# Optimization experiments

Hardware: AMD Instinct MI355X
Metric: run time of the kernel (lower is better)

The kernel has to match this reference:

```python
import jax, jax.numpy as jnp
import numpy as np

N_NODES = 50000
N_EDGES = 800000
FEAT = 128
HID1 = 128
HID2 = 64


def setup_inputs() -> dict:
    key = jax.random.key(0)
    k = jax.random.split(key, 6)
    x = jax.random.normal(k[0], (N_NODES, FEAT), dtype=jnp.float32)
    edge_index = jax.random.randint(k[1], (2, N_EDGES), 0, N_NODES, dtype=jnp.int32)
    # Glorot-style init scaling like PyG's GCNConv linear
    W1 = jax.random.normal(k[2], (FEAT, HID1), dtype=jnp.float32) * (1.0 / np.sqrt(FEAT))
    b1 = jnp.zeros((HID1,), dtype=jnp.float32)
    W2 = jax.random.normal(k[3], (HID1, HID2), dtype=jnp.float32) * (1.0 / np.sqrt(HID1))
    b2 = jnp.zeros((HID2,), dtype=jnp.float32)
    return {"x": x, "edge_index": edge_index, "W1": W1, "b1": b1, "W2": W2, "b2": b2}


def _gcn_conv(x, src, dst, W, b, n_nodes):
    """PyG GCNConv: h = X W; out_i = sum_j norm_ij h_j + b, with self-loops and
    symmetric normalization norm_ij = deg_i^-1/2 * deg_j^-1/2 (deg counts self-loop)."""
    h = x @ W  # [N, out]
    # degree at target nodes (self-loops already appended to src/dst)
    deg = jax.ops.segment_sum(jnp.ones_like(dst, dtype=h.dtype), dst, num_segments=n_nodes)
    dinv = jax.lax.rsqrt(jnp.maximum(deg, 1.0))  # deg >= 1 because of self-loops
    norm = dinv[src] * dinv[dst]  # [E+N]
    msg = h[src] * norm[:, None]  # gather + scale, [E+N, out]
    out = jax.ops.segment_sum(msg, dst, num_segments=n_nodes)
    return out + b


def reference(x, edge_index, W1, b1, W2, b2):
    n = x.shape[0]
    self_idx = jnp.arange(n, dtype=edge_index.dtype)
    src = jnp.concatenate([edge_index[0], self_idx])
    dst = jnp.concatenate([edge_index[1], self_idx])
    h = jax.nn.relu(_gcn_conv(x, src, dst, W1, b1, n))
    out = _gcn_conv(h, src, dst, W2, b2, n)
    return out
```

## Files before the change

kernel.cpp:

```cpp
#include <hip/hip_runtime.h>
#include <hip/hip_bf16.h>


__device__ __forceinline__ float bf_lo(unsigned u) { return __uint_as_float(u << 16); }
__device__ __forceinline__ float bf_hi(unsigned u) { return __uint_as_float(u & 0xffff0000u); }
__device__ __forceinline__ unsigned short f2bf(float f) {
    return (unsigned short)(__bfloat16_as_ushort(__float2bfloat16(f)));
}

__global__ __launch_bounds__(256) void zero_kernel(int* __restrict__ a, int n) {
    int i = blockIdx.x * 256 + threadIdx.x;
    if (i < n) a[i] = 0;
}

__global__ __launch_bounds__(256) void count_kernel(const int* __restrict__ dst,
                                                    int* __restrict__ cnt,
                                                    int* __restrict__ eslot, int E) {
    int e = blockIdx.x * 256 + threadIdx.x;
    if (e < E) eslot[e] = atomicAdd(&cnt[dst[e]], 1);
}

__global__ __launch_bounds__(256) void scan1_kernel(const int* __restrict__ cnt,
                                                    int* __restrict__ row_ptr,
                                                    int* __restrict__ blksum,
                                                    float* __restrict__ dinv, int N) {
    __shared__ int sm[256];
    int i = blockIdx.x * 256 + threadIdx.x;
    int v = (i < N) ? cnt[i] : 0;
    if (i < N) dinv[i] = rsqrtf((float)(v + 1));
    sm[threadIdx.x] = v;
    __syncthreads();
    for (int off = 1; off < 256; off <<= 1) {
        int t = (threadIdx.x >= off) ? sm[threadIdx.x - off] : 0;
        __syncthreads();
        sm[threadIdx.x] += t;
        __syncthreads();
    }
    if (i < N) row_ptr[i] = sm[threadIdx.x] - v;
    if (threadIdx.x == 255) blksum[blockIdx.x] = sm[255];
}

__global__ __launch_bounds__(256) void scan2_kernel(int* __restrict__ blksum, int nb) {
    __shared__ int sm[256];
    int i = threadIdx.x;
    int v = (i < nb) ? blksum[i] : 0;
    sm[i] = v;
    __syncthreads();
    for (int off = 1; off < 256; off <<= 1) {
        int t = (i >= off) ? sm[i - off] : 0;
        __syncthreads();
        sm[i] += t;
        __syncthreads();
    }
    if (i < nb) blksum[i] = sm[i] - v;
}

__global__ __launch_bounds__(256) void scan3_kernel(int* __restrict__ row_ptr,
                                                    const int* __restrict__ blksum,
                                                    int N, int E) {
    int i = blockIdx.x * 256 + threadIdx.x;
    if (i < N) row_ptr[i] += blksum[blockIdx.x];
    if (i == 0) row_ptr[N] = E;
}

__global__ __launch_bounds__(256) void scatter_kernel(const int* __restrict__ src,
                                                      const int* __restrict__ dst,
                                                      const int* __restrict__ row_ptr,
                                                      const int* __restrict__ eslot,
                                                      int* __restrict__ ssrc, int E) {
    int e = blockIdx.x * 256 + threadIdx.x;
    if (e < E) {
        int p = row_ptr[dst[e]] + eslot[e];
        ssrc[p] = src[e];
    }
}

template <int M>
__global__ __launch_bounds__(256) void gemm_kernel(const float* __restrict__ A,
                                                   const float* __restrict__ W,
                                                   const float* __restrict__ dinv,
                                                   unsigned short* __restrict__ C,
                                                   int N) {
    constexpr int K = 128, KC = 32, TN = M / 16;
    __shared__ float As[64][33];
    __shared__ float Bs[KC][M];

    int tid = threadIdx.x;
    int tx = tid & 15;
    int ty = tid >> 4;
    int row0 = blockIdx.x * 64;

    float acc[4][TN];
#pragma unroll
    for (int i = 0; i < 4; ++i)
#pragma unroll
        for (int j = 0; j < TN; ++j) acc[i][j] = 0.f;

    for (int kc = 0; kc < K; kc += KC) {
#pragma unroll
        for (int f = 0; f < 2; ++f) {
            int q = tid + 256 * f;
            int r = q >> 3;
            int kq = (q & 7) << 2;
            int grow = row0 + r;
            float4 v = make_float4(0.f, 0.f, 0.f, 0.f);
            if (grow < N) v = *(const float4*)(A + (size_t)grow * K + kc + kq);
            As[r][kq + 0] = v.x;
            As[r][kq + 1] = v.y;
            As[r][kq + 2] = v.z;
            As[r][kq + 3] = v.w;
        }
        constexpr int BQ = KC * M / 4;
#pragma unroll
        for (int f = 0; f < BQ / 256; ++f) {
            int q = tid + 256 * f;
            int r = q / (M / 4);
            int c4 = (q % (M / 4)) << 2;
            *(float4*)(&Bs[r][c4]) = *(const float4*)(W + (size_t)(kc + r) * M + c4);
        }
        __syncthreads();

#pragma unroll
        for (int k = 0; k < KC; ++k) {
            float a[4], b[TN];
#pragma unroll
            for (int i = 0; i < 4; ++i) a[i] = As[ty * 4 + i][k];
#pragma unroll
            for (int j = 0; j < TN; ++j) b[j] = Bs[k][tx * TN + j];
#pragma unroll
            for (int i = 0; i < 4; ++i)
#pragma unroll
                for (int j = 0; j < TN; ++j) acc[i][j] += a[i] * b[j];
        }
        __syncthreads();
    }

#pragma unroll
    for (int i = 0; i < 4; ++i) {
        int grow = row0 + ty * 4 + i;
        if (grow < N) {
            float dv = dinv[grow];
            unsigned short us[TN];
#pragma unroll
            for (int j = 0; j < TN; ++j) us[j] = f2bf(acc[i][j] * dv);
            if constexpr (TN == 8) {
                uint4 pk;
                pk.x = (unsigned)us[0] | ((unsigned)us[1] << 16);
                pk.y = (unsigned)us[2] | ((unsigned)us[3] << 16);
                pk.z = (unsigned)us[4] | ((unsigned)us[5] << 16);
                pk.w = (unsigned)us[6] | ((unsigned)us[7] << 16);
                *(uint4*)(C + (size_t)grow * M + tx * TN) = pk;
            } else {
                uint2 pk;
                pk.x = (unsigned)us[0] | ((unsigned)us[1] << 16);
                pk.y = (unsigned)us[2] | ((unsigned)us[3] << 16);
                *(uint2*)(C + (size_t)grow * M + tx * TN) = pk;
            }
        }
    }
}

template <int M, bool RELU>
__global__ __launch_bounds__(256) void agg_kernel(const unsigned short* __restrict__ g,
                                                  const int* __restrict__ row_ptr,
                                                  const int* __restrict__ ssrc,
                                                  const float* __restrict__ dinv,
                                                  const float* __restrict__ bias,
                                                  float* __restrict__ out, int N) {
    int node = __builtin_amdgcn_readfirstlane((int)(blockIdx.x * 4 + (threadIdx.x >> 6)));
    if (node >= N) return;
    int lane = threadIdx.x & 63;
    float di = dinv[node];
    int beg = row_ptr[node];
    int end = row_ptr[node + 1];

    if constexpr (M == 128) {
        const unsigned* hp = (const unsigned*)g;
        unsigned hv = hp[node * 64 + lane];
        float ax0 = bf_lo(hv), ay0 = bf_hi(hv);
        float ax1 = 0.f, ay1 = 0.f;
        int j = beg;
        for (; j + 7 < end; j += 8) {
            int s0 = ssrc[j + 0], s1 = ssrc[j + 1], s2 = ssrc[j + 2], s3 = ssrc[j + 3];
            int s4 = ssrc[j + 4], s5 = ssrc[j + 5], s6 = ssrc[j + 6], s7 = ssrc[j + 7];
            unsigned v0 = hp[s0 * 64 + lane], v1 = hp[s1 * 64 + lane];
            unsigned v2 = hp[s2 * 64 + lane], v3 = hp[s3 * 64 + lane];
            unsigned v4 = hp[s4 * 64 + lane], v5 = hp[s5 * 64 + lane];
            unsigned v6 = hp[s6 * 64 + lane], v7 = hp[s7 * 64 + lane];
            ax0 += bf_lo(v0) + bf_lo(v1) + bf_lo(v2) + bf_lo(v3);
            ax1 += bf_lo(v4) + bf_lo(v5) + bf_lo(v6) + bf_lo(v7);
            ay0 += bf_hi(v0) + bf_hi(v1) + bf_hi(v2) + bf_hi(v3);
            ay1 += bf_hi(v4) + bf_hi(v5) + bf_hi(v6) + bf_hi(v7);
        }
        for (; j + 3 < end; j += 4) {
            int s0 = ssrc[j + 0], s1 = ssrc[j + 1], s2 = ssrc[j + 2], s3 = ssrc[j + 3];
            unsigned v0 = hp[s0 * 64 + lane], v1 = hp[s1 * 64 + lane];
            unsigned v2 = hp[s2 * 64 + lane], v3 = hp[s3 * 64 + lane];
            ax0 += bf_lo(v0) + bf_lo(v1);
            ax1 += bf_lo(v2) + bf_lo(v3);
            ay0 += bf_hi(v0) + bf_hi(v1);
            ay1 += bf_hi(v2) + bf_hi(v3);
        }
        for (; j < end; ++j) {
            unsigned v = hp[ssrc[j] * 64 + lane];
            ax0 += bf_lo(v);
            ay0 += bf_hi(v);
        }
        float ax = (ax0 + ax1) * di + bias[2 * lane];
        float ay = (ay0 + ay1) * di + bias[2 * lane + 1];
        if (RELU) { ax = fmaxf(ax, 0.f); ay = fmaxf(ay, 0.f); }
        ((float2*)out)[node * 64 + lane] = make_float2(ax, ay);
    } else {
        float a0 = __uint_as_float((unsigned)g[node * 64 + lane] << 16);
        float a1 = 0.f;
        int j = beg;
        for (; j + 7 < end; j += 8) {
            int s0 = ssrc[j + 0], s1 = ssrc[j + 1], s2 = ssrc[j + 2], s3 = ssrc[j + 3];
            int s4 = ssrc[j + 4], s5 = ssrc[j + 5], s6 = ssrc[j + 6], s7 = ssrc[j + 7];
            float v0 = __uint_as_float((unsigned)g[s0 * 64 + lane] << 16);
            float v1 = __uint_as_float((unsigned)g[s1 * 64 + lane] << 16);
            float v2 = __uint_as_float((unsigned)g[s2 * 64 + lane] << 16);
            float v3 = __uint_as_float((unsigned)g[s3 * 64 + lane] << 16);
            float v4 = __uint_as_float((unsigned)g[s4 * 64 + lane] << 16);
            float v5 = __uint_as_float((unsigned)g[s5 * 64 + lane] << 16);
            float v6 = __uint_as_float((unsigned)g[s6 * 64 + lane] << 16);
            float v7 = __uint_as_float((unsigned)g[s7 * 64 + lane] << 16);
            a0 += v0 + v1 + v2 + v3;
            a1 += v4 + v5 + v6 + v7;
        }
        for (; j + 3 < end; j += 4) {
            int s0 = ssrc[j + 0], s1 = ssrc[j + 1], s2 = ssrc[j + 2], s3 = ssrc[j + 3];
            float v0 = __uint_as_float((unsigned)g[s0 * 64 + lane] << 16);
            float v1 = __uint_as_float((unsigned)g[s1 * 64 + lane] << 16);
            float v2 = __uint_as_float((unsigned)g[s2 * 64 + lane] << 16);
            float v3 = __uint_as_float((unsigned)g[s3 * 64 + lane] << 16);
            a0 += v0 + v1;
            a1 += v2 + v3;
        }
        for (; j < end; ++j)
            a0 += __uint_as_float((unsigned)g[ssrc[j] * 64 + lane] << 16);
        float acc = (a0 + a1) * di + bias[lane];
        if (RELU) acc = fmaxf(acc, 0.f);
        out[node * 64 + lane] = acc;
    }
}

extern "C" void kernel_launch(void* const* d_in, const int* in_sizes, int n_in,
                              void* d_out, int out_size, void* d_ws, size_t ws_size,
                              hipStream_t stream) {
    const float* x = (const float*)d_in[0];
    const int* eidx = (const int*)d_in[1];
    const float* W1 = (const float*)d_in[2];
    const float* b1 = (const float*)d_in[3];
    const float* W2 = (const float*)d_in[4];
    const float* b2 = (const float*)d_in[5];
    float* out = (float*)d_out;

    const int N = in_sizes[0] / 128;
    const int E = in_sizes[1] / 2;
    const int* src = eidx;
    const int* dst = eidx + E;

    char* ws = (char*)d_ws;
    size_t off = 0;
    auto alloc = [&](size_t bytes) -> char* {
        char* p = ws + off;
        off = (off + bytes + 255) & ~(size_t)255;
        return p;
    };
    int* cnt = (int*)alloc((size_t)N * 4);
    int* row_ptr = (int*)alloc((size_t)(N + 1) * 4);
    int* blksum = (int*)alloc(256 * 4);
    int* eslot = (int*)alloc((size_t)E * 4);
    int* ssrc = (int*)alloc((size_t)E * 4);
    float* dinv = (float*)alloc((size_t)N * 4);
    unsigned short* g1 = (unsigned short*)alloc((size_t)N * 128 * 2);
    float* z1 = (float*)alloc((size_t)N * 128 * 4);
    unsigned short* g2 = (unsigned short*)alloc((size_t)N * 64 * 2);

    const int nbN = (N + 255) / 256;
    const int nbE = (E + 255) / 256;

    zero_kernel<<<nbN, 256, 0, stream>>>(cnt, N);
    count_kernel<<<nbE, 256, 0, stream>>>(dst, cnt, eslot, E);
    scan1_kernel<<<nbN, 256, 0, stream>>>(cnt, row_ptr, blksum, dinv, N);
    scan2_kernel<<<1, 256, 0, stream>>>(blksum, nbN);
    scan3_kernel<<<nbN, 256, 0, stream>>>(row_ptr, blksum, N, E);
    scatter_kernel<<<nbE, 256, 0, stream>>>(src, dst, row_ptr, eslot, ssrc, E);

    const int gb = (N + 63) / 64;
    gemm_kernel<128><<<gb, 256, 0, stream>>>(x, W1, dinv, g1, N);
    agg_kernel<128, true><<<(N + 3) / 4, 256, 0, stream>>>(g1, row_ptr, ssrc, dinv, b1, z1, N);
    gemm_kernel<64><<<gb, 256, 0, stream>>>(z1, W2, dinv, g2, N);
    agg_kernel<64, false><<<(N + 3) / 4, 256, 0, stream>>>(g2, row_ptr, ssrc, dinv, b2, out, N);
}
```

Before: 233.1 us.

## Store layer-1 activations in bf16 and restructure GEMM with full-row A tiles

The first aggregation now writes its ReLU output as bf16 instead of fp32, halving the intermediate buffer that the second GEMM reads. The GEMM loads the whole 64x128 A tile into shared memory once, as fp32 or bf16, instead of per K-chunk. Its inner loop is rewritten to use float4 shared-memory reads with an interleaved column mapping for vectorized B access. This trades extra rounding of the hidden activations for less memory traffic, and the larger shared footprint (32KB for fp32 A) may reduce occupancy.

New measurement: 243.7 us. 1.05x slower.

```diff
diff --git a/kernel.cpp b/kernel.cpp
--- a/kernel.cpp
+++ b/kernel.cpp
@@ -75,41 +75,55 @@
     }
 }
 
-template <int M>
-__global__ __launch_bounds__(256) void gemm_kernel(const float* __restrict__ A,
+template <int M, bool ABF16>
+__global__ __launch_bounds__(256) void gemm_kernel(const void* __restrict__ Araw,
                                                    const float* __restrict__ W,
                                                    const float* __restrict__ dinv,
                                                    unsigned short* __restrict__ C,
                                                    int N) {
-    constexpr int K = 128, KC = 32, TN = M / 16;
-    __shared__ float As[64][33];
+    constexpr int K = 128, KC = 32, TN = M / 16, NH = M / 64;
     __shared__ float Bs[KC][M];
-
-    int tid = threadIdx.x;
-    int tx = tid & 15;
-    int ty = tid >> 4;
-    int row0 = blockIdx.x * 64;
-
-    float acc[4][TN];
-#pragma unroll
-    for (int i = 0; i < 4; ++i)
-#pragma unroll
-        for (int j = 0; j < TN; ++j) acc[i][j] = 0.f;
-
-    for (int kc = 0; kc < K; kc += KC) {
-#pragma unroll
-        for (int f = 0; f < 2; ++f) {
+    __shared__ float AsF[ABF16 ? 1 : 64 * K];
+    __shared__ unsigned short AsH[ABF16 ? 64 * K : 1];
+
+    const int tid = threadIdx.x;
+    const int tx = tid & 15;
+    const int ty = tid >> 4;
+    const int row0 = blockIdx.x * 64;
+
+    if constexpr (!ABF16) {
+        const float* A = (const float*)Araw;
+#pragma unroll
+        for (int f = 0; f < 8; ++f) {
             int q = tid + 256 * f;
-            int r = q >> 3;
-            int kq = (q & 7) << 2;
+            int r = q >> 5;
+            int c4 = (q & 31) << 2;
             int grow = row0 + r;
             float4 v = make_float4(0.f, 0.f, 0.f, 0.f);
-            if (grow < N) v = *(const float4*)(A + (size_t)grow * K + kc + kq);
-            As[r][kq + 0] = v.x;
-            As[r][kq + 1] = v.y;
-            As[r][kq + 2] = v.z;
-            As[r][kq + 3] = v.w;
-        }
+            if (grow < N) v = *(const float4*)(A + (size_t)grow * K + c4);
+            *(float4*)&AsF[r * K + c4] = v;
+        }
+    } else {
+        const unsigned short* A = (const unsigned short*)Araw;
+#pragma unroll
+        for (int f = 0; f < 4; ++f) {
+            int q = tid + 256 * f;
+            int r = q >> 4;
+            int ch = q & 15;
+            int grow = row0 + r;
+            uint4 v = {0u, 0u, 0u, 0u};
+            if (grow < N) v = *(const uint4*)(A + (size_t)grow * K + ch * 8);
+            *(uint4*)&AsH[r * K + ch * 8] = v;
+        }
+    }
+
+    float acc[4][TN];
+#pragma unroll
+    for (int i = 0; i < 4; ++i)
+#pragma unroll
+        for (int j = 0; j < TN; ++j) acc[i][j] = 0.f;
+
+    for (int kc = 0; kc < K; kc += KC) {
         constexpr int BQ = KC * M / 4;
 #pragma unroll
         for (int f = 0; f < BQ / 256; ++f) {
@@ -120,17 +134,67 @@
         }
         __syncthreads();
 
-#pragma unroll
-        for (int k = 0; k < KC; ++k) {
-            float a[4], b[TN];
-#pragma unroll
-            for (int i = 0; i < 4; ++i) a[i] = As[ty * 4 + i][k];
-#pragma unroll
-            for (int j = 0; j < TN; ++j) b[j] = Bs[k][tx * TN + j];
-#pragma unroll
-            for (int i = 0; i < 4; ++i)
-#pragma unroll
-                for (int j = 0; j < TN; ++j) acc[i][j] += a[i] * b[j];
+        if constexpr (!ABF16) {
+#pragma unroll
+            for (int k4 = 0; k4 < KC / 4; ++k4) {
+                int kk = kc + k4 * 4;
+                float4 a4[4];
+#pragma unroll
+                for (int i = 0; i < 4; ++i)
+                    a4[i] = *(const float4*)&AsF[(ty * 4 + i) * K + kk];
+#pragma unroll
+                for (int k2 = 0; k2 < 4; ++k2) {
+                    int kl = k4 * 4 + k2;
+                    float4 b[NH];
+#pragma unroll
+                    for (int h = 0; h < NH; ++h)
+                        b[h] = *(const float4*)&Bs[kl][h * 64 + tx * 4];
+#pragma unroll
+                    for (int i = 0; i < 4; ++i) {
+                        float a = ((const float*)&a4[i])[k2];
+#pragma unroll
+                        for (int h = 0; h < NH; ++h) {
+                            acc[i][h * 4 + 0] += a * b[h].x;
+                            acc[i][h * 4 + 1] += a * b[h].y;
+                            acc[i][h * 4 + 2] += a * b[h].z;
+                            acc[i][h * 4 + 3] += a * b[h].w;
+                        }
+                    }
+                }
+            }
+        } else {
+#pragma unroll
+            for (int k8 = 0; k8 < KC / 8; ++k8) {
+                int kk = kc + k8 * 8;
+                float a[4][8];
+#pragma unroll
+                for (int i = 0; i < 4; ++i) {
+                    uint4 u = *(const uint4*)&AsH[(ty * 4 + i) * K + kk];
+                    a[i][0] = bf_lo(u.x); a[i][1] = bf_hi(u.x);
+                    a[i][2] = bf_lo(u.y); a[i][3] = bf_hi(u.y);
+                    a[i][4] = bf_lo(u.z); a[i][5] = bf_hi(u.z);
+                    a[i][6] = bf_lo(u.w); a[i][7] = bf_hi(u.w);
+                }
+#pragma unroll
+                for (int k2 = 0; k2 < 8; ++k2) {
+                    int kl = k8 * 8 + k2;
+                    float4 b[NH];
+#pragma unroll
+                    for (int h = 0; h < NH; ++h)
+                        b[h] = *(const float4*)&Bs[kl][h * 64 + tx * 4];
+#pragma unroll
+                    for (int i = 0; i < 4; ++i) {
+                        float av = a[i][k2];
+#pragma unroll
+                        for (int h = 0; h < NH; ++h) {
+                            acc[i][h * 4 + 0] += av * b[h].x;
+                            acc[i][h * 4 + 1] += av * b[h].y;
+                            acc[i][h * 4 + 2] += av * b[h].z;
+                            acc[i][h * 4 + 3] += av * b[h].w;
+                        }
+                    }
+                }
+            }
         }
         __syncthreads();
     }
@@ -140,33 +204,28 @@
         int grow = row0 + ty * 4 + i;
         if (grow < N) {
             float dv = dinv[grow];
-            unsigned short us[TN];
-#pragma unroll
-            for (int j = 0; j < TN; ++j) us[j] = f2bf(acc[i][j] * dv);
-            if constexpr (TN == 8) {
-                uint4 pk;
-                pk.x = (unsigned)us[0] | ((unsigned)us[1] << 16);
-                pk.y = (unsigned)us[2] | ((unsigned)us[3] << 16);
-                pk.z = (unsigned)us[4] | ((unsigned)us[5] << 16);
-                pk.w = (unsigned)us[6] | ((unsigned)us[7] << 16);
-                *(uint4*)(C + (size_t)grow * M + tx * TN) = pk;
-            } else {
+#pragma unroll
+            for (int h = 0; h < NH; ++h) {
+                unsigned short u0 = f2bf(acc[i][h * 4 + 0] * dv);
+                unsigned short u1 = f2bf(acc[i][h * 4 + 1] * dv);
+                unsigned short u2 = f2bf(acc[i][h * 4 + 2] * dv);
+                unsigned short u3 = f2bf(acc[i][h * 4 + 3] * dv);
                 uint2 pk;
-                pk.x = (unsigned)us[0] | ((unsigned)us[1] << 16);
-                pk.y = (unsigned)us[2] | ((unsigned)us[3] << 16);
-                *(uint2*)(C + (size_t)grow * M + tx * TN) = pk;
+                pk.x = (unsigned)u0 | ((unsigned)u1 << 16);
+                pk.y = (unsigned)u2 | ((unsigned)u3 << 16);
+                *(uint2*)(C + (size_t)grow * M + h * 64 + tx * 4) = pk;
             }
         }
     }
 }
 
-template <int M, bool RELU>
+template <int M, bool RELU, bool OUTBF16>
 __global__ __launch_bounds__(256) void agg_kernel(const unsigned short* __restrict__ g,
                                                   const int* __restrict__ row_ptr,
                                                   const int* __restrict__ ssrc,
                                                   const float* __restrict__ dinv,
                                                   const float* __restrict__ bias,
-                                                  float* __restrict__ out, int N) {
+                                                  void* __restrict__ outraw, int N) {
     int node = __builtin_amdgcn_readfirstlane((int)(blockIdx.x * 4 + (threadIdx.x >> 6)));
     if (node >= N) return;
     int lane = threadIdx.x & 63;
@@ -209,7 +268,12 @@
         float ax = (ax0 + ax1) * di + bias[2 * lane];
         float ay = (ay0 + ay1) * di + bias[2 * lane + 1];
         if (RELU) { ax = fmaxf(ax, 0.f); ay = fmaxf(ay, 0.f); }
-        ((float2*)out)[node * 64 + lane] = make_float2(ax, ay);
+        if constexpr (OUTBF16) {
+            unsigned pk = (unsigned)f2bf(ax) | ((unsigned)f2bf(ay) << 16);
+            ((unsigned*)outraw)[node * 64 + lane] = pk;
+        } else {
+            ((float2*)outraw)[node * 64 + lane] = make_float2(ax, ay);
+        }
     } else {
         float a0 = __uint_as_float((unsigned)g[node * 64 + lane] << 16);
         float a1 = 0.f;
@@ -241,7 +305,11 @@
             a0 += __uint_as_float((unsigned)g[ssrc[j] * 64 + lane] << 16);
         float acc = (a0 + a1) * di + bias[lane];
         if (RELU) acc = fmaxf(acc, 0.f);
-        out[node * 64 + lane] = acc;
+        if constexpr (OUTBF16) {
+            ((unsigned short*)outraw)[node * 64 + lane] = f2bf(acc);
+        } else {
+            ((float*)outraw)[node * 64 + lane] = acc;
+        }
     }
 }
 
@@ -275,7 +343,7 @@
     int* ssrc = (int*)alloc((size_t)E * 4);
     float* dinv = (float*)alloc((size_t)N * 4);
     unsigned short* g1 = (unsigned short*)alloc((size_t)N * 128 * 2);
-    float* z1 = (float*)alloc((size_t)N * 128 * 4);
+    unsigned short* z1 = (unsigned short*)alloc((size_t)N * 128 * 2);
     unsigned short* g2 = (unsigned short*)alloc((size_t)N * 64 * 2);
 
     const int nbN = (N + 255) / 256;
@@ -289,8 +357,8 @@
     scatter_kernel<<<nbE, 256, 0, stream>>>(src, dst, row_ptr, eslot, ssrc, E);
 
     const int gb = (N + 63) / 64;
-    gemm_kernel<128><<<gb, 256, 0, stream>>>(x, W1, dinv, g1, N);
-    agg_kernel<128, true><<<(N + 3) / 4, 256, 0, stream>>>(g1, row_ptr, ssrc, dinv, b1, z1, N);
-    gemm_kernel<64><<<gb, 256, 0, stream>>>(z1, W2, dinv, g2, N);
-    agg_kernel<64, false><<<(N + 3) / 4, 256, 0, stream>>>(g2, row_ptr, ssrc, dinv, b2, out, N);
-}
+    gemm_kernel<128, false><<<gb, 256, 0, stream>>>(x, W1, dinv, g1, N);
+    agg_kernel<128, true, true><<<(N + 3) / 4, 256, 0, stream>>>(g1, row_ptr, ssrc, dinv, b1, z1, N);
+    gemm_kernel<64, true><<<gb, 256, 0, stream>>>(z1, W2, dinv, g2, N);
+    agg_kernel<64, false, false><<<(N + 3) / 4, 256, 0, stream>>>(g2, row_ptr, ssrc, dinv, b2, out, N);
+}
```

## Use bf16 MFMA for dense GEMMs and store hidden layer in bf16

Applied to the files above, without the earlier changes.

Replaces the FP32 shared-memory tiled GEMM with a register-only bf16 MFMA kernel (16x16x32). The weights are pre-packed into a bf16 fragment layout by a small kernel. The first aggregation now writes its ReLU output in bf16, which halves the intermediate traffic and lets the second GEMM load A fragments directly. The cost is two extra launches, narrow 2-byte scattered output stores, and lower precision in the intermediate activations.

Result: faster. 210.5 us (-9.7%).

```diff
diff --git a/kernel.cpp b/kernel.cpp
--- a/kernel.cpp
+++ b/kernel.cpp
@@ -1,6 +1,9 @@
 #include <hip/hip_runtime.h>
 #include <hip/hip_bf16.h>
 
+
+typedef __attribute__((ext_vector_type(8))) short short8;
+typedef __attribute__((ext_vector_type(4))) float f32x4;
 
 __device__ __forceinline__ float bf_lo(unsigned u) { return __uint_as_float(u << 16); }
 __device__ __forceinline__ float bf_hi(unsigned u) { return __uint_as_float(u & 0xffff0000u); }
@@ -75,98 +78,96 @@
     }
 }
 
-template <int M>
-__global__ __launch_bounds__(256) void gemm_kernel(const float* __restrict__ A,
-                                                   const float* __restrict__ W,
-                                                   const float* __restrict__ dinv,
-                                                   unsigned short* __restrict__ C,
-                                                   int N) {
-    constexpr int K = 128, KC = 32, TN = M / 16;
-    __shared__ float As[64][33];
-    __shared__ float Bs[KC][M];
-
-    int tid = threadIdx.x;
-    int tx = tid & 15;
-    int ty = tid >> 4;
-    int row0 = blockIdx.x * 64;
-
-    float acc[4][TN];
-#pragma unroll
-    for (int i = 0; i < 4; ++i)
-#pragma unroll
-        for (int j = 0; j < TN; ++j) acc[i][j] = 0.f;
-
-    for (int kc = 0; kc < K; kc += KC) {
-#pragma unroll
-        for (int f = 0; f < 2; ++f) {
-            int q = tid + 256 * f;
-            int r = q >> 3;
-            int kq = (q & 7) << 2;
-            int grow = row0 + r;
-            float4 v = make_float4(0.f, 0.f, 0.f, 0.f);
-            if (grow < N) v = *(const float4*)(A + (size_t)grow * K + kc + kq);
-            As[r][kq + 0] = v.x;
-            As[r][kq + 1] = v.y;
-            As[r][kq + 2] = v.z;
-            As[r][kq + 3] = v.w;
-        }
-        constexpr int BQ = KC * M / 4;
-#pragma unroll
-        for (int f = 0; f < BQ / 256; ++f) {
-            int q = tid + 256 * f;
-            int r = q / (M / 4);
-            int c4 = (q % (M / 4)) << 2;
-            *(float4*)(&Bs[r][c4]) = *(const float4*)(W + (size_t)(kc + r) * M + c4);
-        }
-        __syncthreads();
-
-#pragma unroll
-        for (int k = 0; k < KC; ++k) {
-            float a[4], b[TN];
-#pragma unroll
-            for (int i = 0; i < 4; ++i) a[i] = As[ty * 4 + i][k];
-#pragma unroll
-            for (int j = 0; j < TN; ++j) b[j] = Bs[k][tx * TN + j];
-#pragma unroll
-            for (int i = 0; i < 4; ++i)
-#pragma unroll
-                for (int j = 0; j < TN; ++j) acc[i][j] += a[i] * b[j];
-        }
-        __syncthreads();
-    }
-
-#pragma unroll
-    for (int i = 0; i < 4; ++i) {
-        int grow = row0 + ty * 4 + i;
-        if (grow < N) {
-            float dv = dinv[grow];
-            unsigned short us[TN];
-#pragma unroll
-            for (int j = 0; j < TN; ++j) us[j] = f2bf(acc[i][j] * dv);
-            if constexpr (TN == 8) {
-                uint4 pk;
-                pk.x = (unsigned)us[0] | ((unsigned)us[1] << 16);
-                pk.y = (unsigned)us[2] | ((unsigned)us[3] << 16);
-                pk.z = (unsigned)us[4] | ((unsigned)us[5] << 16);
-                pk.w = (unsigned)us[6] | ((unsigned)us[7] << 16);
-                *(uint4*)(C + (size_t)grow * M + tx * TN) = pk;
-            } else {
-                uint2 pk;
-                pk.x = (unsigned)us[0] | ((unsigned)us[1] << 16);
-                pk.y = (unsigned)us[2] | ((unsigned)us[3] << 16);
-                *(uint2*)(C + (size_t)grow * M + tx * TN) = pk;
-            }
-        }
-    }
-}
-
-template <int M, bool RELU>
+__global__ __launch_bounds__(256) void packw_kernel(const float* __restrict__ W,
+                                                    unsigned short* __restrict__ Wp,
+                                                    int ncol) {
+    int i = blockIdx.x * 256 + threadIdx.x;
+    if (i < 128 * ncol) {
+        int j = i & 7;
+        int n = (i >> 3) % ncol;
+        int kb = i / (8 * ncol);
+        Wp[i] = f2bf(W[(kb * 8 + j) * ncol + n]);
+    }
+}
+
+template <int M, bool ABF16>
+__global__ __launch_bounds__(256) void mfma_gemm_kernel(const void* __restrict__ Araw,
+                                                        const unsigned short* __restrict__ Wp,
+                                                        const float* __restrict__ dinv,
+                                                        unsigned short* __restrict__ C,
+                                                        int N) {
+    constexpr int NT = M / 16;
+    const int lane = threadIdx.x & 63;
+    const int wave = threadIdx.x >> 6;
+    const int col = lane & 15;
+    const int quad = lane >> 4;
+    const int row0w = (blockIdx.x * 4 + wave) * 16;
+
+    int arow = row0w + col;
+    if (arow >= N) arow = N - 1;
+
+    short8 afr[4];
+    if constexpr (!ABF16) {
+        const float* Xr = (const float*)Araw + (size_t)arow * 128;
+#pragma unroll
+        for (int c = 0; c < 4; ++c) {
+            float4 f0 = *(const float4*)(Xr + c * 32 + quad * 8);
+            float4 f1 = *(const float4*)(Xr + c * 32 + quad * 8 + 4);
+            short8 a;
+            a[0] = (short)f2bf(f0.x); a[1] = (short)f2bf(f0.y);
+            a[2] = (short)f2bf(f0.z); a[3] = (short)f2bf(f0.w);
+            a[4] = (short)f2bf(f1.x); a[5] = (short)f2bf(f1.y);
+            a[6] = (short)f2bf(f1.z); a[7] = (short)f2bf(f1.w);
+            afr[c] = a;
+        }
+    } else {
+        const uint4* Z = (const uint4*)Araw;
+#pragma unroll
+        for (int c = 0; c < 4; ++c) {
+            union { uint4 u; short8 s; } cv;
+            cv.u = Z[(size_t)arow * 16 + c * 4 + quad];
+            afr[c] = cv.s;
+        }
+    }
+
+    f32x4 acc[NT];
+#pragma unroll
+    for (int t = 0; t < NT; ++t) acc[t] = (f32x4){0.f, 0.f, 0.f, 0.f};
+
+    const uint4* Wq = (const uint4*)Wp;
+#pragma unroll
+    for (int c = 0; c < 4; ++c) {
+        short8 bfr[NT];
+#pragma unroll
+        for (int t = 0; t < NT; ++t) {
+            union { uint4 u; short8 s; } cv;
+            cv.u = Wq[(size_t)(c * 4 + quad) * M + t * 16 + col];
+            bfr[t] = cv.s;
+        }
+#pragma unroll
+        for (int t = 0; t < NT; ++t)
+            acc[t] = __builtin_amdgcn_mfma_f32_16x16x32_bf16(afr[c], bfr[t], acc[t], 0, 0, 0);
+    }
+
+#pragma unroll
+    for (int r = 0; r < 4; ++r) {
+        int row = row0w + quad * 4 + r;
+        if (row < N) {
+            float dv = dinv[row];
+#pragma unroll
+            for (int t = 0; t < NT; ++t)
+                C[(size_t)row * M + t * 16 + col] = f2bf(acc[t][r] * dv);
+        }
+    }
+}
+
+template <int M, bool RELU, bool OUTBF16>
 __global__ __launch_bounds__(256) void agg_kernel(const unsigned short* __restrict__ g,
                                                   const int* __restrict__ row_ptr,
                                                   const int* __restrict__ ssrc,
                                                   const float* __restrict__ dinv,
                                                   const float* __restrict__ bias,
-                                                  float* __restrict__ out, int N) {
+                                                  void* __restrict__ outraw, int N) {
     int node = __builtin_amdgcn_readfirstlane((int)(blockIdx.x * 4 + (threadIdx.x >> 6)));
     if (node >= N) return;
     int lane = threadIdx.x & 63;
@@ -209,7 +210,12 @@
         float ax = (ax0 + ax1) * di + bias[2 * lane];
         float ay = (ay0 + ay1) * di + bias[2 * lane + 1];
         if (RELU) { ax = fmaxf(ax, 0.f); ay = fmaxf(ay, 0.f); }
-        ((float2*)out)[node * 64 + lane] = make_float2(ax, ay);
+        if constexpr (OUTBF16) {
+            unsigned pk = (unsigned)f2bf(ax) | ((unsigned)f2bf(ay) << 16);
+            ((unsigned*)outraw)[node * 64 + lane] = pk;
+        } else {
+            ((float2*)outraw)[node * 64 + lane] = make_float2(ax, ay);
+        }
     } else {
         float a0 = __uint_as_float((unsigned)g[node * 64 + lane] << 16);
         float a1 = 0.f;
@@ -241,7 +247,11 @@
             a0 += __uint_as_float((unsigned)g[ssrc[j] * 64 + lane] << 16);
         float acc = (a0 + a1) * di + bias[lane];
         if (RELU) acc = fmaxf(acc, 0.f);
-        out[node * 64 + lane] = acc;
+        if constexpr (OUTBF16) {
+            ((unsigned short*)outraw)[node * 64 + lane] = f2bf(acc);
+        } else {
+            ((float*)outraw)[node * 64 + lane] = acc;
+        }
     }
 }
 
@@ -274,8 +284,10 @@
     int* eslot = (int*)alloc((size_t)E * 4);
     int* ssrc = (int*)alloc((size_t)E * 4);
     float* dinv = (float*)alloc((size_t)N * 4);
+    unsigned short* Wp1 = (unsigned short*)alloc(128 * 128 * 2);
+    unsigned short* Wp2 = (unsigned short*)alloc(128 * 64 * 2);
     unsigned short* g1 = (unsigned short*)alloc((size_t)N * 128 * 2);
-    float* z1 = (float*)alloc((size_t)N * 128 * 4);
+    unsigned short* z1 = (unsigned short*)alloc((size_t)N * 128 * 2);
     unsigned short* g2 = (unsigned short*)alloc((size_t)N * 64 * 2);
 
     const int nbN = (N + 255) / 256;
@@ -288,9 +300,12 @@
     scan3_kernel<<<nbN, 256, 0, stream>>>(row_ptr, blksum, N, E);
     scatter_kernel<<<nbE, 256, 0, stream>>>(src, dst, row_ptr, eslot, ssrc, E);
 
+    packw_kernel<<<(128 * 128 + 255) / 256, 256, 0, stream>>>(W1, Wp1, 128);
+    packw_kernel<<<(128 * 64 + 255) / 256, 256, 0, stream>>>(W2, Wp2, 64);
+
     const int gb = (N + 63) / 64;
-    gemm_kernel<128><<<gb, 256, 0, stream>>>(x, W1, dinv, g1, N);
-    agg_kernel<128, true><<<(N + 3) / 4, 256, 0, stream>>>(g1, row_ptr, ssrc, dinv, b1, z1, N);
-    gemm_kernel<64><<<gb, 256, 0, stream>>>(z1, W2, dinv, g2, N);
-    agg_kernel<64, false><<<(N + 3) / 4, 256, 0, stream>>>(g2, row_ptr, ssrc, dinv, b2, out, N);
-}
+    mfma_gemm_kernel<128, false><<<gb, 256, 0, stream>>>(x, Wp1, dinv, g1, N);
+    agg_kernel<128, true, true><<<(N + 3) / 4, 256, 0, stream>>>(g1, row_ptr, ssrc, dinv, b1, z1, N);
+    mfma_gemm_kernel<64, true><<<gb, 256, 0, stream>>>(z1, Wp2, dinv, g2, N);
+    agg_kernel<64, false, false><<<(N + 3) / 4, 256, 0, stream>>>(g2, row_ptr, ssrc, dinv, b2, out, N);
+}
```
